# Kernel optimization log

Measured on AMD Instinct MI355X. Metric: run time of the kernel, lower is better.

## Reference

```python
import jax, jax.numpy as jnp
import numpy as np

N_NODES = 1_000_000
N_EDGES = 16_000_000
N_IN, HID, N_OUT = 128, 32, 16


def setup_inputs() -> dict:
    key = jax.random.key(0)
    ks = jax.random.split(key, 8)
    x = jax.random.normal(ks[0], (N_NODES, N_IN), dtype=jnp.float32)
    edge_index = jax.random.randint(ks[1], (2, N_EDGES), 0, N_NODES, dtype=jnp.int64)
    edge_weight = jax.random.uniform(ks[2], (N_EDGES,), dtype=jnp.float32)
    # ChebConv(K=1) parameters: one linear per layer + bias
    def glorot(k, fan_in, fan_out):
        s = jnp.sqrt(6.0 / (fan_in + fan_out))
        return jax.random.uniform(k, (fan_in, fan_out), minval=-s, maxval=s, dtype=jnp.float32)
    W0 = glorot(ks[3], N_IN, HID)
    b0 = jnp.zeros((HID,), dtype=jnp.float32)
    W1 = glorot(ks[4], HID, HID)
    b1 = jnp.zeros((HID,), dtype=jnp.float32)
    W2 = glorot(ks[5], HID, N_OUT)
    b2 = jnp.zeros((N_OUT,), dtype=jnp.float32)
    return {"x": x, "edge_index": edge_index, "edge_weight": edge_weight,
            "W0": W0, "b0": b0, "W1": W1, "b1": b1, "W2": W2, "b2": b2}


def reference(x, edge_index, edge_weight, W0, b0, W1, b1, W2, b2):
    # PyG ChebConv with K=1: out = lins[0](Tx_0) + bias, Tx_0 = x.
    # The Laplacian propagation over edge_index/edge_weight is only used for K>=2,
    # so edge_index/edge_weight do not enter the math (kept for signature fidelity).
    h = jax.nn.relu(x @ W0 + b0)      # ChebConv1 + relu
    h = jax.nn.relu(h @ W1 + b1)      # ChebConv2 + relu
    # Dropout(p=0.0) is identity
    return h @ W2 + b2                # ChebConv3 -> [N, nOutputs]
```

## Files before the change

kernel.cpp:

```cpp
#include <hip/hip_runtime.h>
#include <stdint.h>


#define N_IN  128
#define HID   32
#define N_OUT 16

using f32x4  = __attribute__((ext_vector_type(4))) float;
using short8 = __attribute__((ext_vector_type(8))) short;
using uint4v = __attribute__((ext_vector_type(4))) unsigned int;

#define N_CHUNKS 22
#define TOTAL_WF_SHORTS (N_CHUNKS * 512)
#define WLDS_GRANULES (N_CHUNKS * 64)

__device__ __forceinline__ unsigned fu(float f) {
    union { float f; unsigned u; } v; v.f = f; return v.u;
}
__device__ __forceinline__ float uf(unsigned u) {
    union { unsigned u; float f; } v; v.u = u; return v.f;
}
__device__ __forceinline__ unsigned short f2bf_rne(float f) {
    unsigned u = fu(f);
    return (unsigned short)((u + 0x7fffu + ((u >> 16) & 1u)) >> 16);
}

__global__ void split_weights(const float* __restrict__ W0,
                              const float* __restrict__ W1,
                              const float* __restrict__ W2,
                              unsigned short* __restrict__ wf) {
    int idx = blockIdx.x * blockDim.x + threadIdx.x;
    if (idx >= TOTAL_WF_SHORTS) return;
    int chunk  = idx >> 9;
    int within = idx & 511;
    int lane = within >> 3;
    int j    = within & 7;
    int g4   = 4 * (lane >> 4);
    int r16  = lane & 15;
    int rho  = (j < 4) ? (g4 + j) : (16 + g4 + (j - 4));
    float v; int hl;
    if (chunk < 16) {
        int kc = chunk >> 2, b = (chunk >> 1) & 1; hl = chunk & 1;
        int k = kc * 32 + 2 * g4 + j;
        v = W0[k * HID + 16 * b + r16];
    } else if (chunk < 20) {
        int c2 = chunk - 16, b = c2 >> 1; hl = c2 & 1;
        v = W1[rho * HID + 16 * b + r16];
    } else {
        hl = chunk - 20;
        v = W2[rho * N_OUT + r16];
    }
    unsigned hi_bits = fu(v) & 0xFFFF0000u;
    wf[idx] = (hl == 0) ? (unsigned short)(hi_bits >> 16)
                        : f2bf_rne(v - uf(hi_bits));
}

#define MFMA3(acc, wh, wl, xh, xl)                                          \
    do {                                                                    \
        acc = __builtin_amdgcn_mfma_f32_16x16x32_bf16(wh, xh, acc, 0, 0, 0);\
        acc = __builtin_amdgcn_mfma_f32_16x16x32_bf16(wl, xh, acc, 0, 0, 0);\
        acc = __builtin_amdgcn_mfma_f32_16x16x32_bf16(wh, xl, acc, 0, 0, 0);\
    } while (0)

#define SPLIT8A(farr, AH, AL)                                               \
    do {                                                                    \
        uint4v hv_, lv_;                                                    \
        _Pragma("unroll")                                                   \
        for (int p_ = 0; p_ < 4; ++p_) {                                    \
            unsigned u0_ = fu((farr)[2 * p_]), u1_ = fu((farr)[2 * p_ + 1]);\
            unsigned h0_ = u0_ & 0xFFFF0000u, h1_ = u1_ & 0xFFFF0000u;      \
            hv_[p_] = h1_ | (u0_ >> 16);                                    \
            float l0_ = (farr)[2 * p_] - uf(h0_);                           \
            float l1_ = (farr)[2 * p_ + 1] - uf(h1_);                       \
            lv_[p_] = (fu(l1_) & 0xFFFF0000u) | (fu(l0_) >> 16);            \
        }                                                                   \
        AH = __builtin_bit_cast(short8, hv_);                               \
        AL = __builtin_bit_cast(short8, lv_);                               \
    } while (0)

#define GAS1(p) ((const unsigned int __attribute__((address_space(1)))*)(uintptr_t)(p))
#define LAS3(p) ((unsigned int __attribute__((address_space(3)))*)(uintptr_t)(p))

__global__ __launch_bounds__(256, 1) void gnn_mfma(
    const float* __restrict__ x, const unsigned short* __restrict__ wf,
    const float* __restrict__ b0, const float* __restrict__ b1,
    const float* __restrict__ b2, float* __restrict__ out,
    int n_tiles, int stride)
{
    __shared__ __align__(16) unsigned short wlds[N_CHUNKS * 512];
    __shared__ __align__(16) float xbuf[4][2][2048];

    const int tid  = threadIdx.x;
    const int wave = tid >> 6;
    const int l    = tid & 63;
    const int r16  = l & 15;
    const int g    = l >> 4;

    {
        const uint4v* wfv = reinterpret_cast<const uint4v*>(wf);
        uint4v* wl = reinterpret_cast<uint4v*>(wlds);
        for (int gg = tid; gg < WLDS_GRANULES; gg += 256)
            wl[gg] = wfv[gg];
    }
    __syncthreads();

    const short8* WL = reinterpret_cast<const short8*>(wlds);

    const f32x4 bb0a = *reinterpret_cast<const f32x4*>(b0 + 4 * g);
    const f32x4 bb0b = *reinterpret_cast<const f32x4*>(b0 + 16 + 4 * g);
    const f32x4 bb1a = *reinterpret_cast<const f32x4*>(b1 + 4 * g);
    const f32x4 bb1b = *reinterpret_cast<const f32x4*>(b1 + 16 + 4 * g);
    const f32x4 bb2  = *reinterpret_cast<const f32x4*>(b2 + 4 * g);

    const int gw = blockIdx.x * 4 + wave;

    const int srow = l >> 5;
    const int st   = l & 31;

    #define STAGE(buf, tileidx)                                                \
    do {                                                                       \
        const float* sb_ = x + (size_t)(tileidx) * 16 * N_IN;                  \
        _Pragma("unroll")                                                      \
        for (int i_ = 0; i_ < 8; ++i_) {                                       \
            int row_ = i_ * 2 + srow;                                          \
            const float* src_ = sb_ + row_ * N_IN + ((st ^ row_) << 2);        \
            float* dst_ = &xbuf[wave][buf][i_ * 256];                          \
            __builtin_amdgcn_global_load_lds(GAS1(src_), LAS3(dst_), 16, 0, 0);\
        }                                                                      \
    } while (0)

    int b = 0;
    STAGE(0, gw);

    for (int tile = gw; tile < n_tiles; tile += stride) {
        const int nb = tile * 16;

        asm volatile("s_waitcnt vmcnt(0)" ::: "memory");
        __builtin_amdgcn_sched_barrier(0);

        f32x4 xa[4], xbv[4];
        {
            const f32x4* rb = reinterpret_cast<const f32x4*>(&xbuf[wave][b][r16 * 128]);
            #pragma unroll
            for (int kc = 0; kc < 4; ++kc) {
                int t0 = g * 2 + kc * 8;
                xa[kc]  = rb[t0 ^ r16];
                xbv[kc] = rb[(t0 + 1) ^ r16];
            }
        }

        {
            int ntt = tile + stride;
            int pf = (ntt < n_tiles) ? ntt : tile;
            STAGE(b ^ 1, pf);
        }

        f32x4 acc0 = {0.f, 0.f, 0.f, 0.f};
        f32x4 acc1 = {0.f, 0.f, 0.f, 0.f};

        #pragma unroll
        for (int kc = 0; kc < 4; ++kc) {
            float f[8] = {xa[kc][0], xa[kc][1], xa[kc][2], xa[kc][3],
                          xbv[kc][0], xbv[kc][1], xbv[kc][2], xbv[kc][3]};
            short8 xh, xl;
            SPLIT8A(f, xh, xl);
            short8 w0h0 = WL[(kc * 4 + 0) * 64 + l];
            short8 w0l0 = WL[(kc * 4 + 1) * 64 + l];
            short8 w0h1 = WL[(kc * 4 + 2) * 64 + l];
            short8 w0l1 = WL[(kc * 4 + 3) * 64 + l];
            MFMA3(acc0, w0h0, w0l0, xh, xl);
            MFMA3(acc1, w0h1, w0l1, xh, xl);
        }

        float hf[8];
        #pragma unroll
        for (int i = 0; i < 4; ++i) {
            hf[i]     = fmaxf(acc0[i] + bb0a[i], 0.f);
            hf[4 + i] = fmaxf(acc1[i] + bb0b[i], 0.f);
        }
        short8 hbh, hbl;
        SPLIT8A(hf, hbh, hbl);

        f32x4 acc2 = {0.f, 0.f, 0.f, 0.f};
        f32x4 acc3 = {0.f, 0.f, 0.f, 0.f};
        {
            short8 w1h0 = WL[(16 + 0) * 64 + l];
            short8 w1l0 = WL[(16 + 1) * 64 + l];
            short8 w1h1 = WL[(16 + 2) * 64 + l];
            short8 w1l1 = WL[(16 + 3) * 64 + l];
            MFMA3(acc2, w1h0, w1l0, hbh, hbl);
            MFMA3(acc3, w1h1, w1l1, hbh, hbl);
        }
        float hf2[8];
        #pragma unroll
        for (int i = 0; i < 4; ++i) {
            hf2[i]     = fmaxf(acc2[i] + bb1a[i], 0.f);
            hf2[4 + i] = fmaxf(acc3[i] + bb1b[i], 0.f);
        }
        short8 h2h, h2l;
        SPLIT8A(hf2, h2h, h2l);

        f32x4 accO = {0.f, 0.f, 0.f, 0.f};
        {
            short8 w2h = WL[(20) * 64 + l];
            short8 w2l = WL[(21) * 64 + l];
            MFMA3(accO, w2h, w2l, h2h, h2l);
        }

        f32x4 ov;
        #pragma unroll
        for (int i = 0; i < 4; ++i) ov[i] = accO[i] + bb2[i];
        __builtin_nontemporal_store(
            ov, reinterpret_cast<f32x4*>(out + (size_t)(nb + r16) * N_OUT + 4 * g));

        b ^= 1;
    }
    #undef STAGE
}

extern "C" void kernel_launch(void* const* d_in, const int* in_sizes, int n_in,
                              void* d_out, int out_size, void* d_ws, size_t ws_size,
                              hipStream_t stream) {
    const float* x  = (const float*)d_in[0];
    const float* W0 = (const float*)d_in[3];
    const float* b0 = (const float*)d_in[4];
    const float* W1 = (const float*)d_in[5];
    const float* b1 = (const float*)d_in[6];
    const float* W2 = (const float*)d_in[7];
    const float* b2 = (const float*)d_in[8];
    float* out = (float*)d_out;
    unsigned short* wf = (unsigned short*)d_ws;

    int n_nodes = in_sizes[0] / N_IN;
    int n_tiles = n_nodes / 16;

    split_weights<<<(TOTAL_WF_SHORTS + 255) / 256, 256, 0, stream>>>(W0, W1, W2, wf);

    const int n_blocks = 256;
    const int n_waves_total = n_blocks * 4;
    gnn_mfma<<<dim3(n_blocks), dim3(256), 0, stream>>>(
        x, wf, b0, b1, b2, out, n_tiles, n_waves_total);
}
```

Baseline: 111.1 us.

## Hold split weights in registers and double grid with two blocks per CU

Each lane now loads its 22 weight fragments straight from global memory into registers, replacing the per-block LDS copy, the block barrier and the per-tile LDS weight reads. Freeing that LDS together with launch_bounds(256,2) allows two blocks per CU, and the grid doubles to 512 blocks to raise the number of waves in flight for this memory-bound stream. The cost is 88 extra VGPRs per lane, which could pressure the register budget under the tighter launch bound. A guard also skips the initial prefetch for waves that have no tile.

```diff
diff --git a/kernel.cpp b/kernel.cpp
--- a/kernel.cpp
+++ b/kernel.cpp
@@ -12,7 +12,6 @@
 
 #define N_CHUNKS 22
 #define TOTAL_WF_SHORTS (N_CHUNKS * 512)
-#define WLDS_GRANULES (N_CHUNKS * 64)
 
 __device__ __forceinline__ unsigned fu(float f) {
     union { float f; unsigned u; } v; v.f = f; return v.u;
@@ -81,13 +80,12 @@
 #define GAS1(p) ((const unsigned int __attribute__((address_space(1)))*)(uintptr_t)(p))
 #define LAS3(p) ((unsigned int __attribute__((address_space(3)))*)(uintptr_t)(p))
 
-__global__ __launch_bounds__(256, 1) void gnn_mfma(
+__global__ __launch_bounds__(256, 2) void gnn_mfma(
     const float* __restrict__ x, const unsigned short* __restrict__ wf,
     const float* __restrict__ b0, const float* __restrict__ b1,
     const float* __restrict__ b2, float* __restrict__ out,
     int n_tiles, int stride)
 {
-    __shared__ __align__(16) unsigned short wlds[N_CHUNKS * 512];
     __shared__ __align__(16) float xbuf[4][2][2048];
 
     const int tid  = threadIdx.x;
@@ -96,15 +94,13 @@
     const int r16  = l & 15;
     const int g    = l >> 4;
 
+    short8 W[N_CHUNKS];
     {
-        const uint4v* wfv = reinterpret_cast<const uint4v*>(wf);
-        uint4v* wl = reinterpret_cast<uint4v*>(wlds);
-        for (int gg = tid; gg < WLDS_GRANULES; gg += 256)
-            wl[gg] = wfv[gg];
+        const short8* WF = reinterpret_cast<const short8*>(wf);
+        #pragma unroll
+        for (int c = 0; c < N_CHUNKS; ++c)
+            W[c] = WF[c * 64 + l];
     }
-    __syncthreads();
-
-    const short8* WL = reinterpret_cast<const short8*>(wlds);
 
     const f32x4 bb0a = *reinterpret_cast<const f32x4*>(b0 + 4 * g);
     const f32x4 bb0b = *reinterpret_cast<const f32x4*>(b0 + 16 + 4 * g);
@@ -130,7 +126,7 @@
     } while (0)
 
     int b = 0;
-    STAGE(0, gw);
+    if (gw < n_tiles) STAGE(0, gw);
 
     for (int tile = gw; tile < n_tiles; tile += stride) {
         const int nb = tile * 16;
@@ -164,12 +160,8 @@
                           xbv[kc][0], xbv[kc][1], xbv[kc][2], xbv[kc][3]};
             short8 xh, xl;
             SPLIT8A(f, xh, xl);
-            short8 w0h0 = WL[(kc * 4 + 0) * 64 + l];
-            short8 w0l0 = WL[(kc * 4 + 1) * 64 + l];
-            short8 w0h1 = WL[(kc * 4 + 2) * 64 + l];
-            short8 w0l1 = WL[(kc * 4 + 3) * 64 + l];
-            MFMA3(acc0, w0h0, w0l0, xh, xl);
-            MFMA3(acc1, w0h1, w0l1, xh, xl);
+            MFMA3(acc0, W[kc * 4 + 0], W[kc * 4 + 1], xh, xl);
+            MFMA3(acc1, W[kc * 4 + 2], W[kc * 4 + 3], xh, xl);
         }
 
         float hf[8];
@@ -183,14 +175,9 @@
 
         f32x4 acc2 = {0.f, 0.f, 0.f, 0.f};
         f32x4 acc3 = {0.f, 0.f, 0.f, 0.f};
-        {
-            short8 w1h0 = WL[(16 + 0) * 64 + l];
-            short8 w1l0 = WL[(16 + 1) * 64 + l];
-            short8 w1h1 = WL[(16 + 2) * 64 + l];
-            short8 w1l1 = WL[(16 + 3) * 64 + l];
-            MFMA3(acc2, w1h0, w1l0, hbh, hbl);
-            MFMA3(acc3, w1h1, w1l1, hbh, hbl);
-        }
+        MFMA3(acc2, W[16], W[17], hbh, hbl);
+        MFMA3(acc3, W[18], W[19], hbh, hbl);
+
         float hf2[8];
         #pragma unroll
         for (int i = 0; i < 4; ++i) {
@@ -201,11 +188,7 @@
         SPLIT8A(hf2, h2h, h2l);
 
         f32x4 accO = {0.f, 0.f, 0.f, 0.f};
-        {
-            short8 w2h = WL[(20) * 64 + l];
-            short8 w2l = WL[(21) * 64 + l];
-            MFMA3(accO, w2h, w2l, h2h, h2l);
-        }
+        MFMA3(accO, W[20], W[21], h2h, h2l);
 
         f32x4 ov;
         #pragma unroll
@@ -236,7 +219,7 @@
 
     split_weights<<<(TOTAL_WF_SHORTS + 255) / 256, 256, 0, stream>>>(W0, W1, W2, wf);
 
-    const int n_blocks = 256;
+    const int n_blocks = 512;
     const int n_waves_total = n_blocks * 4;
     gnn_mfma<<<dim3(n_blocks), dim3(256), 0, stream>>>(
         x, wf, b0, b1, b2, out, n_tiles, n_waves_total);
```

Result: slower. 119.0 us (+7.1%).
